# Kernel optimization log

Hardware: AMD Instinct MI355X
Metric: run time of the kernel (lower is better)

## Reference

```python
import jax, jax.numpy as jnp
import numpy as np
import math

PAD_IDX = 1
BOS_IDX = 2
B, S, T = 32, 128, 64
E, H, L, V = 256, 512, 2, 32000


def _lstm_cell(gates, c):
    # torch gate order: i, f, g, o
    i, f, g, o = jnp.split(gates, 4, axis=-1)
    c_new = jax.nn.sigmoid(f) * c + jax.nn.sigmoid(i) * jnp.tanh(g)
    h_new = jax.nn.sigmoid(o) * jnp.tanh(c_new)
    return h_new, c_new


def _run_lstm_layer(x_tbi, Wih, Whh, b, h0, c0):
    def step(carry, x_t):
        h, c = carry
        h2, c2 = _lstm_cell(x_t @ Wih + h @ Whh + b, c)
        return (h2, c2), h2
    (hT, cT), ys = jax.lax.scan(step, (h0, c0), x_tbi)
    return ys, hT, cT


def setup_inputs() -> dict:
    key = jax.random.key(0)
    ks = iter(jax.random.split(key, 40))
    def w(shape, s=0.05):
        return jax.random.normal(next(ks), shape, jnp.float32) * s
    inp = {
        'src_tokens': jax.random.randint(next(ks), (B, S), 0, V, dtype=jnp.int32),
        'tgt_tokens': jax.random.randint(next(ks), (B, T), 0, V, dtype=jnp.int32),
        'src_emb': w((V, E), 0.02),
        'tgt_emb': w((V, E), 0.02),
        'enc_Wih0': w((E, 4 * H)), 'enc_Whh0': w((H, 4 * H)), 'enc_b0': jnp.zeros((4 * H,), jnp.float32),
        'enc_Wih1': w((H, 4 * H)), 'enc_Whh1': w((H, 4 * H)), 'enc_b1': jnp.zeros((4 * H,), jnp.float32),
        'dec_Wih0': w((E + H, 4 * H)), 'dec_Whh0': w((H, 4 * H)), 'dec_b0': jnp.zeros((4 * H,), jnp.float32),
        'dec_Wih1': w((H, 4 * H)), 'dec_Whh1': w((H, 4 * H)), 'dec_b1': jnp.zeros((4 * H,), jnp.float32),
        'attn_W': w((2 * H, H)), 'attn_b': jnp.zeros((H,), jnp.float32),
        'v_w': w((H,)),
        'coal_w': w((L, 1), 0.5), 'coal_b': jnp.zeros((1,), jnp.float32),
        'out_W': w((2 * H + E, V)), 'out_b': jnp.zeros((V,), jnp.float32),
    }
    return inp


def reference(src_tokens, tgt_tokens, src_emb, tgt_emb,
              enc_Wih0, enc_Whh0, enc_b0, enc_Wih1, enc_Whh1, enc_b1,
              dec_Wih0, dec_Whh0, dec_b0, dec_Wih1, dec_Whh1, dec_b1,
              attn_W, attn_b, v_w, coal_w, coal_b, out_W, out_b):
    Bq = src_tokens.shape[0]
    sqrtE_src = np.float32(math.sqrt(src_emb.shape[1]))
    sqrtE_tgt = np.float32(math.sqrt(tgt_emb.shape[1]))

    # ---- Encoder (2-layer LSTM, batch_first; dropout=0 eval) ----
    x = (src_emb[src_tokens] * sqrtE_src).transpose(1, 0, 2)  # (S,B,E)
    z = jnp.zeros((Bq, H), jnp.float32)
    ys0, hA, cA = _run_lstm_layer(x, enc_Wih0, enc_Whh0, enc_b0, z, z)
    ys1, hB, cB = _run_lstm_layer(ys0, enc_Wih1, enc_Whh1, enc_b1, z, z)
    enc_out = ys1.transpose(1, 0, 2)          # (B,S,H)
    hidden = jnp.stack([hA, hB])              # (L,B,H)
    cell = jnp.stack([cA, cB])

    mask = src_tokens != PAD_IDX              # (B,S)
    Wq, We = attn_W[:H], attn_W[H:]
    enc_proj = enc_out @ We                   # (B,S,H) loop-invariant part of attn linear

    def dec_step(carry, tok):
        h, c = carry                          # (L,B,H) each
        emb = jax.nn.relu(tgt_emb[tok] * sqrtE_tgt)          # (B,E)
        # faithful raw reshape (L,B,H) -> (B,H,L), coalesce layers
        q = jax.nn.relu(h.reshape(Bq, H, L) @ coal_w + coal_b)[..., 0]  # (B,H)
        e = jnp.tanh(enc_proj + (q @ Wq + attn_b)[:, None, :])          # (B,S,H)
        score = e @ v_w                                                 # (B,S)
        score = jnp.where(mask, score, np.float32(-1e10))
        a = jax.nn.softmax(score, axis=1)
        wctx = jnp.einsum('bs,bsh->bh', a, enc_out)                     # (B,H)
        xin = jnp.concatenate([emb, wctx], axis=-1)                     # (B,E+H)
        h0n, c0n = _lstm_cell(xin @ dec_Wih0 + h[0] @ dec_Whh0 + dec_b0, c[0])
        h1n, c1n = _lstm_cell(h0n @ dec_Wih1 + h[1] @ dec_Whh1 + dec_b1, c[1])
        logits = jnp.concatenate([h1n, wctx, emb], axis=-1) @ out_W + out_b  # (B,V)
        return (jnp.stack([h0n, h1n]), jnp.stack([c0n, c1n])), logits

    (hF, cF), outs = jax.lax.scan(dec_step, (hidden, cell), tgt_tokens[:, :-1].T)
    first = jnp.full((Bq, 1, out_b.shape[0]), np.float32(BOS_IDX))  # decoder_outputs[:,0]=BOS_IDX
    dec_outputs = jnp.concatenate([first, outs.transpose(1, 0, 2)], axis=1)  # (B,T,V)
    return dec_outputs, hF, cF
```

## Files before the change

### kernel.cpp

```cpp
#include <hip/hip_runtime.h>
#include <hip/hip_bf16.h>

typedef __bf16 bf16x8 __attribute__((ext_vector_type(8)));
typedef float f32x4 __attribute__((ext_vector_type(4)));
typedef unsigned long long u64;

#define DEV static __device__ __forceinline__

constexpr int Bq = 32, Sq = 128, Tq = 64, Eq = 256, Hq = 512, Vq = 32000;
constexpr int G4 = 2048;
constexpr int TD = 63;
constexpr int KOUT = 1280;
constexpr float SQRTE = 16.0f;

DEV float sigf(float x) { return 1.0f / (1.0f + __expf(-x)); }
DEV float tanh_fast(float x) {
    float ax = fabsf(x);
    float t = __expf(-2.f * ax);
    float r = (1.f - t) / (1.f + t);
    return x < 0.f ? -r : r;
}
DEV float tanh_c(float x) {
    float xc = fminf(fmaxf(x, -15.f), 15.f);
    float t = __expf(2.f * xc);
    return (t - 1.f) / (t + 1.f);
}

DEV u64 ldc(const u64* p) {
    return __hip_atomic_load(p, __ATOMIC_RELAXED, __HIP_MEMORY_SCOPE_AGENT);
}
DEV unsigned ldc32(const unsigned* p) {
    return __hip_atomic_load(p, __ATOMIC_RELAXED, __HIP_MEMORY_SCOPE_AGENT);
}
DEV void stc(u64* p, u64 v) {
    __hip_atomic_store(p, v, __ATOMIC_RELAXED, __HIP_MEMORY_SCOPE_AGENT);
}
DEV void stc32(unsigned* p, unsigned v) {
    __hip_atomic_store(p, v, __ATOMIC_RELAXED, __HIP_MEMORY_SCOPE_AGENT);
}
DEV unsigned short bfbits(float f) {
    __bf16 h = (__bf16)f;
    return __builtin_bit_cast(unsigned short, h);
}
DEV float bf2f(unsigned short u) {
    __bf16 h = __builtin_bit_cast(__bf16, u);
    return (float)h;
}
DEV u64 pack4bf(float a, float b, float c, float d) {
    return (u64)bfbits(a) | ((u64)bfbits(b) << 16) |
           ((u64)bfbits(c) << 32) | ((u64)bfbits(d) << 48);
}
DEV u64 pack2f(float a, float b) {
    return (u64)__float_as_uint(a) | ((u64)__float_as_uint(b) << 32);
}

DEV void gbar(unsigned* flags, int nblk, unsigned epoch) {
    __syncthreads();
    if (threadIdx.x < 64) {
        if (threadIdx.x == 0) {
            asm volatile("s_waitcnt vmcnt(0)" ::: "memory");
            stc32(flags + blockIdx.x * 32, epoch);
        }
        int lane = threadIdx.x;
        for (;;) {
            unsigned v = (lane < nblk) ? ldc32(flags + lane * 32) : 0xffffffffu;
            if (__all((int)(v >= epoch))) break;
            __builtin_amdgcn_s_sleep(1);
        }
    }
    __syncthreads();
}

__global__ __launch_bounds__(256) void k_embed_src(const int* __restrict__ tok,
                                                   const float* __restrict__ emb,
                                                   __hip_bfloat16* __restrict__ x)
{
    int idx = blockIdx.x * 256 + threadIdx.x;
    int e = idx & (Eq - 1);
    int r = idx >> 8;
    int b = r & 31, t = r >> 5;
    x[idx] = __float2bfloat16(emb[(size_t)tok[b * Sq + t] * Eq + e] * SQRTE);
}

__global__ __launch_bounds__(256) void k_embed_tgt(const int* __restrict__ tok,
                                                   const float* __restrict__ emb,
                                                   __hip_bfloat16* __restrict__ embt,
                                                   __hip_bfloat16* __restrict__ Xout)
{
    int idx = blockIdx.x * 256 + threadIdx.x;
    int e = idx & (Eq - 1);
    int r = idx >> 8;
    int b = r & 31, t = r >> 5;
    float v = fmaxf(0.f, emb[(size_t)tok[b * Tq + t] * Eq + e] * SQRTE);
    embt[idx] = __float2bfloat16(v);
    Xout[(size_t)r * KOUT + 1024 + e] = __float2bfloat16(v);
}

__global__ __launch_bounds__(256) void k_transpose_bf16(const float* __restrict__ W,
                                                        __hip_bfloat16* __restrict__ Wt,
                                                        int K, int N)
{
    __shared__ float tile[32][33];
    int nb = blockIdx.x * 32, kb = blockIdx.y * 32;
    int c = threadIdx.x & 31, r4 = threadIdx.x >> 5;
    for (int i = 0; i < 32; i += 8)
        tile[r4 + i][c] = W[(size_t)(kb + r4 + i) * N + nb + c];
    __syncthreads();
    for (int i = 0; i < 32; i += 8) {
        int rr = r4 + i;
        Wt[(size_t)(nb + rr) * K + kb + c] = __float2bfloat16(tile[c][rr]);
    }
}

DEV void stage_coh(const u64* src, __bf16* As) {
    int tx = threadIdx.x;
#pragma unroll
    for (int p = 0; p < 8; ++p) {
        int c = tx + p * 256;
        int row = c >> 6, kc = c & 63;
        u64 v0 = ldc(src + c * 2);
        u64 v1 = ldc(src + c * 2 + 1);
        int kd = kc ^ (row & 7);
        *(u64*)(As + row * 512 + kd * 8) = v0;
        *(u64*)(As + row * 512 + kd * 8 + 4) = v1;
    }
}

DEV void mfma_pass(const __bf16* As, const unsigned short* BT, int colB,
                   int kg, int fr, f32x4* acc) {
    const unsigned short* bp = BT + (size_t)colB * 512 + kg * 8;
    int f7 = fr & 7;
#pragma unroll
    for (int k0 = 0; k0 < 512; k0 += 32) {
        int cidx = ((k0 >> 3) | kg) ^ f7;
        bf16x8 bfv = *(const bf16x8*)(bp + k0);
        bf16x8 af0 = *(const bf16x8*)(As + fr * 512 + cidx * 8);
        bf16x8 af1 = *(const bf16x8*)(As + (16 + fr) * 512 + cidx * 8);
        acc[0] = __builtin_amdgcn_mfma_f32_16x16x32_bf16(af0, bfv, acc[0], 0, 0, 0);
        acc[1] = __builtin_amdgcn_mfma_f32_16x16x32_bf16(af1, bfv, acc[1], 0, 0, 0);
    }
}

DEV void mfma_gates(const __bf16* As0, const __bf16* As1,
                    const __hip_bfloat16* B0T, const __hip_bfloat16* B1T,
                    int j0, float* gbuf)
{
    int tx = threadIdx.x, w = tx >> 6, lane = tx & 63;
    int fr = lane & 15, kg = lane >> 4;
    int colB = w * 512 + j0 + fr;
    f32x4 acc[2];
    acc[0] = (f32x4){0.f, 0.f, 0.f, 0.f};
    acc[1] = (f32x4){0.f, 0.f, 0.f, 0.f};
    mfma_pass(As0, (const unsigned short*)B0T, colB, kg, fr, acc);
    if (B1T) mfma_pass(As1, (const unsigned short*)B1T, colB, kg, fr, acc);
    __syncthreads();
    float* gw = gbuf + w * 512;
#pragma unroll
    for (int m = 0; m < 2; ++m)
#pragma unroll
        for (int qd = 0; qd < 4; ++qd)
            gw[(m * 16 + kg * 4 + qd) * 16 + fr] = acc[m][qd];
    __syncthreads();
}

DEV void cell_epi(const float* gbuf, const __hip_bfloat16* xpart, const float* bias,
                  float* cbuf, u64* hb, u64* hf,
                  __hip_bfloat16* eb, int ebs, bool ebcoh,
                  int j0)
{
    int tx = threadIdx.x;
    if (tx >= 128) return;
    int b = tx >> 2, jg = tx & 3;
    int jj0 = jg * 4;
    int j = j0 + jj0;
    float g[4][4];
#pragma unroll
    for (int gi = 0; gi < 4; ++gi) {
        float4 gv = *(const float4*)(gbuf + gi * 512 + b * 16 + jj0);
        g[gi][0] = gv.x; g[gi][1] = gv.y; g[gi][2] = gv.z; g[gi][3] = gv.w;
        if (xpart) {
            u64 xv = *(const u64*)((const unsigned short*)xpart + b * 2048 + gi * 512 + j);
#pragma unroll
            for (int e = 0; e < 4; ++e)
                g[gi][e] += bf2f((unsigned short)(xv >> (16 * e)));
        }
        if (bias) {
            float4 bv = *(const float4*)(bias + gi * 512 + j);
            g[gi][0] += bv.x; g[gi][1] += bv.y; g[gi][2] += bv.z; g[gi][3] += bv.w;
        }
    }
    float4 cv = *(float4*)(cbuf + b * 512 + j);
    float cc[4] = {cv.x, cv.y, cv.z, cv.w};
    float hv[4];
#pragma unroll
    for (int e = 0; e < 4; ++e) {
        float cn = sigf(g[1][e]) * cc[e] + sigf(g[0][e]) * tanh_fast(g[2][e]);
        cc[e] = cn;
        hv[e] = sigf(g[3][e]) * tanh_fast(cn);
    }
    *(float4*)(cbuf + b * 512 + j) = make_float4(cc[0], cc[1], cc[2], cc[3]);
    u64 hpk = pack4bf(hv[0], hv[1], hv[2], hv[3]);
    stc(hb + ((b * 512 + j) >> 2), hpk);
    stc(hf + ((b * 512 + j) >> 1), pack2f(hv[0], hv[1]));
    stc(hf + ((b * 512 + j) >> 1) + 1, pack2f(hv[2], hv[3]));
    if (eb) {
        if (ebcoh) stc((u64*)(eb + (size_t)b * ebs + j), hpk);
        else       *(u64*)(eb + (size_t)b * ebs + j) = hpk;
    }
}

__global__ __launch_bounds__(256) void k_enc_persist(
    const __hip_bfloat16* __restrict__ X0b,
    const __hip_bfloat16* __restrict__ eWhh0T, const __hip_bfloat16* __restrict__ eWih1T,
    const __hip_bfloat16* __restrict__ eWhh1T, const float* __restrict__ eb1,
    __hip_bfloat16* __restrict__ h0b, __hip_bfloat16* __restrict__ h1b,
    float* __restrict__ h0f, float* __restrict__ h1f,
    float* __restrict__ c0, float* __restrict__ c1,
    __hip_bfloat16* __restrict__ ys0b,
    __hip_bfloat16* __restrict__ encb,
    unsigned* __restrict__ flags)
{
    __shared__ __align__(16) char shm[65536];
    __bf16* As0 = (__bf16*)shm;
    __bf16* As1 = (__bf16*)(shm + 32768);
    bool lay1 = blockIdx.x >= 32;
    int j0 = (blockIdx.x & 31) * 16;
    for (int t = 0; t <= 128; ++t) {
        if (!lay1) {
            if (t < 128) {
                stage_coh((const u64*)(h0b + (t & 1) * 16384), As0);
                __syncthreads();
                mfma_gates(As0, nullptr, eWhh0T, nullptr, j0, (float*)As0);
                cell_epi((float*)As0, X0b + (size_t)t * 32 * 2048, nullptr,
                         c0, (u64*)(h0b + ((t + 1) & 1) * 16384), (u64*)h0f,
                         ys0b + (size_t)t * 16384, 512, true, j0);
            }
        } else {
            if (t >= 1) {
                int s = t - 1;
                stage_coh((const u64*)(ys0b + (size_t)s * 16384), As0);
                stage_coh((const u64*)(h1b + (s & 1) * 16384), As1);
                __syncthreads();
                mfma_gates(As0, As1, eWih1T, eWhh1T, j0, (float*)As0);
                cell_epi((float*)As0, nullptr, eb1,
                         c1, (u64*)(h1b + ((s + 1) & 1) * 16384), (u64*)h1f,
                         encb + s * 512, 128 * 512, false, j0);
            }
        }
        gbar(flags, 64, (unsigned)(t + 1));
    }
}

__global__ __launch_bounds__(256) void k_dec_persist(
    const __hip_bfloat16* __restrict__ enc_projb, const __hip_bfloat16* __restrict__ enc_outb,
    const int* __restrict__ src_tok, const float* __restrict__ v_w,
    const __hip_bfloat16* __restrict__ WqT, const float* __restrict__ attn_b,
    const float* __restrict__ coal_w, const float* __restrict__ coal_b,
    const __hip_bfloat16* __restrict__ dWih0wT, const __hip_bfloat16* __restrict__ dWhh0T,
    const __hip_bfloat16* __restrict__ dWih1T, const __hip_bfloat16* __restrict__ dWhh1T,
    const float* __restrict__ db1, const __hip_bfloat16* __restrict__ Xembb,
    float* __restrict__ h0fd, float* __restrict__ h1fd,
    __hip_bfloat16* __restrict__ h0bd, __hip_bfloat16* __restrict__ h1bd,
    float* __restrict__ c0d, float* __restrict__ c1d,
    __hip_bfloat16* __restrict__ wctxb,
    __hip_bfloat16* __restrict__ Xout,
    unsigned* __restrict__ flags)
{
    __shared__ __align__(16) char shm[65536];
    __shared__ float rinvs;
    __bf16* As0 = (__bf16*)shm;
    __bf16* As1 = (__bf16*)(shm + 32768);
    int bid = blockIdx.x, tx = threadIdx.x;
    unsigned bep = 0;

    for (int t = 0; t < TD; ++t) {
        int cur = t & 1, nxt = cur ^ 1;
        __hip_bfloat16* XoutT = Xout + (size_t)t * 32 * KOUT;

        {
            int b = bid;
            float* q   = (float*)shm;
            float* aqs = q + 512;
            float* vws = aqs + 512;
            float* ws  = vws + 512;
            const float* hrow = (b < 16) ? (h0fd + cur * 16384 + b * 1024)
                                         : (h1fd + cur * 16384 + (b - 16) * 1024);
            float cw0 = coal_w[0], cw1 = coal_w[1], cb = coal_b[0];
            for (int j = tx; j < 512; j += 256) {
                u64 pv = ldc((const u64*)hrow + j);
                float v0 = __uint_as_float((unsigned)(pv & 0xffffffffu));
                float v1 = __uint_as_float((unsigned)(pv >> 32));
                q[j] = fmaxf(0.f, v0 * cw0 + v1 * cw1 + cb);
            }
            for (int i = tx; i < 512; i += 256) vws[i] = v_w[i];
            __syncthreads();
            float a0 = attn_b[tx], a1 = attn_b[tx + 256];
            const unsigned short* w0 = (const unsigned short*)WqT + (size_t)tx * 512;
            const unsigned short* w1 = w0 + 256 * 512;
#pragma unroll 4
            for (int j8 = 0; j8 < 512; j8 += 8) {
                bf16x8 wa = *(const bf16x8*)(w0 + j8);
                bf16x8 wb = *(const bf16x8*)(w1 + j8);
#pragma unroll
                for (int e = 0; e < 8; ++e) {
                    float qe = q[j8 + e];
                    a0 += qe * (float)wa[e];
                    a1 += qe * (float)wb[e];
                }
            }
            aqs[tx] = a0; aqs[tx + 256] = a1;
            __syncthreads();
            int s = tx >> 1, half = tx & 1;
            const unsigned short* epr = (const unsigned short*)enc_projb
                                        + ((size_t)(b * 128 + s)) * 512 + half * 256;
            float s0 = 0.f, s1 = 0.f, s2 = 0.f, s3 = 0.f;
#pragma unroll 4
            for (int ii = 0; ii < 256; ii += 8) {
                bf16x8 f8 = *(const bf16x8*)(epr + ii);
                int ib = half * 256 + ii;
                s0 += tanh_c((float)f8[0] + aqs[ib])     * vws[ib];
                s1 += tanh_c((float)f8[1] + aqs[ib + 1]) * vws[ib + 1];
                s2 += tanh_c((float)f8[2] + aqs[ib + 2]) * vws[ib + 2];
                s3 += tanh_c((float)f8[3] + aqs[ib + 3]) * vws[ib + 3];
                s0 += tanh_c((float)f8[4] + aqs[ib + 4]) * vws[ib + 4];
                s1 += tanh_c((float)f8[5] + aqs[ib + 5]) * vws[ib + 5];
                s2 += tanh_c((float)f8[6] + aqs[ib + 6]) * vws[ib + 6];
                s3 += tanh_c((float)f8[7] + aqs[ib + 7]) * vws[ib + 7];
            }
            float p = (s0 + s1) + (s2 + s3);
            p += __shfl_xor(p, 1, 64);
            if (half == 0)
                ws[s] = (src_tok[b * 128 + s] != 1) ? __expf(p) : 0.f;
            __syncthreads();
            if (tx < 64) {
                float ss = ws[tx] + ws[tx + 64];
#pragma unroll
                for (int o = 32; o > 0; o >>= 1) ss += __shfl_down(ss, o, 64);
                if (tx == 0) rinvs = 1.0f / ss;
            }
            __syncthreads();
            float rinv = rinvs;
            const unsigned short* eo = (const unsigned short*)enc_outb + (size_t)b * 65536;
            int i0 = tx * 2;
            float c0a = 0.f, c1a = 0.f;
#pragma unroll 4
            for (int s2i = 0; s2i < 128; ++s2i) {
                unsigned pk2 = *(const unsigned*)(eo + (size_t)s2i * 512 + i0);
                float wv = ws[s2i];
                c0a += wv * bf2f((unsigned short)(pk2 & 0xffffu));
                c1a += wv * bf2f((unsigned short)(pk2 >> 16));
            }
            c0a *= rinv; c1a *= rinv;
            unsigned pk = (unsigned)bfbits(c0a) | ((unsigned)bfbits(c1a) << 16);
            stc32((unsigned*)wctxb + ((b * 512 + i0) >> 1), pk);
            *((unsigned*)XoutT + (((size_t)b * KOUT + 512 + i0) >> 1)) = pk;
        }
        gbar(flags, 32, ++bep);

        {
            int j0 = bid * 16;
            stage_coh((const u64*)wctxb, As0);
            stage_coh((const u64*)(h0bd + cur * 16384), As1);
            __syncthreads();
            mfma_gates(As0, As1, dWih0wT, dWhh0T, j0, (float*)As0);
            cell_epi((float*)As0, Xembb + (size_t)t * 32 * 2048, nullptr,
                     c0d, (u64*)(h0bd + nxt * 16384), (u64*)(h0fd + nxt * 16384),
                     nullptr, 0, false, j0);
        }
        gbar(flags, 32, ++bep);

        {
            int j0 = bid * 16;
            stage_coh((const u64*)(h0bd + nxt * 16384), As0);
            stage_coh((const u64*)(h1bd + cur * 16384), As1);
            __syncthreads();
            mfma_gates(As0, As1, dWih1T, dWhh1T, j0, (float*)As0);
            cell_epi((float*)As0, nullptr, db1,
                     c1d, (u64*)(h1bd + nxt * 16384), (u64*)(h1fd + nxt * 16384),
                     XoutT, KOUT, false, j0);
        }
        gbar(flags, 32, ++bep);
    }
}

__global__ __launch_bounds__(256) void k_mfma(
    const __hip_bfloat16* __restrict__ A, const __hip_bfloat16* __restrict__ BT,
    const float* __restrict__ bias, float* __restrict__ Cf,
    __hip_bfloat16* __restrict__ Cb, int M, int N, int K)
{
    __shared__ __bf16 As[128][72];
    __shared__ __bf16 Bs[128][72];
    const unsigned short* Aw = (const unsigned short*)A;
    const unsigned short* Bw = (const unsigned short*)BT;
    int n0 = blockIdx.x * 128, m0 = blockIdx.y * 128;
    int tx = threadIdx.x;
    int w = tx >> 6, lane = tx & 63;
    int wm = (w >> 1) * 64, wn = (w & 1) * 64;
    int fr = lane & 15, kg = lane >> 4;
    f32x4 acc[4][4];
#pragma unroll
    for (int mi = 0; mi < 4; mi++)
#pragma unroll
        for (int ni = 0; ni < 4; ni++) acc[mi][ni] = (f32x4){0.f, 0.f, 0.f, 0.f};

    for (int k0 = 0; k0 < K; k0 += 64) {
        __syncthreads();
#pragma unroll
        for (int p = 0; p < 4; p++) {
            int ch = tx + p * 256;
            int r = ch >> 3, cc = (ch & 7) * 8;
            uint4 va = {0u, 0u, 0u, 0u};
            int m = m0 + r;
            if (m < M) va = *(const uint4*)(Aw + (size_t)m * K + k0 + cc);
            *(uint4*)(&As[r][cc]) = va;
            uint4 vb = *(const uint4*)(Bw + (size_t)(n0 + r) * K + k0 + cc);
            *(uint4*)(&Bs[r][cc]) = vb;
        }
        __syncthreads();
#pragma unroll
        for (int kk = 0; kk < 64; kk += 32) {
            bf16x8 af[4], bfv[4];
#pragma unroll
            for (int i = 0; i < 4; i++) {
                af[i]  = *(const bf16x8*)(&As[wm + i * 16 + fr][kk + kg * 8]);
                bfv[i] = *(const bf16x8*)(&Bs[wn + i * 16 + fr][kk + kg * 8]);
            }
#pragma unroll
            for (int mi = 0; mi < 4; mi++)
#pragma unroll
                for (int ni = 0; ni < 4; ni++)
                    acc[mi][ni] = __builtin_amdgcn_mfma_f32_16x16x32_bf16(
                        af[mi], bfv[ni], acc[mi][ni], 0, 0, 0);
        }
    }
#pragma unroll
    for (int ni = 0; ni < 4; ni++) {
        int n = n0 + wn + ni * 16 + fr;
        float bv = bias ? bias[n] : 0.f;
#pragma unroll
        for (int mi = 0; mi < 4; mi++) {
#pragma unroll
            for (int qd = 0; qd < 4; qd++) {
                int R = m0 + wm + mi * 16 + kg * 4 + qd;
                if (R < M) {
                    float v = acc[mi][ni][qd] + bv;
                    if (Cf) Cf[(size_t)R * N + n] = v;
                    else    Cb[(size_t)R * N + n] = __float2bfloat16(v);
                }
            }
        }
    }
}

__global__ __launch_bounds__(256) void k_init_dec(
    const float* __restrict__ h0e, const float* __restrict__ h1e,
    const float* __restrict__ c0e, const float* __restrict__ c1e,
    float* __restrict__ h0fd, float* __restrict__ h1fd,
    __hip_bfloat16* __restrict__ h0bd, __hip_bfloat16* __restrict__ h1bd,
    float* __restrict__ c0d, float* __restrict__ c1d)
{
    int idx = blockIdx.x * 256 + threadIdx.x;
    float a = h0e[idx], b = h1e[idx];
    h0fd[idx] = a; h1fd[idx] = b;
    h0bd[idx] = __float2bfloat16(a);
    h1bd[idx] = __float2bfloat16(b);
    c0d[idx] = c0e[idx];
    c1d[idx] = c1e[idx];
}

__global__ __launch_bounds__(256) void k_bos(float* __restrict__ out)
{
    int b = blockIdx.y;
    int i = blockIdx.x * 256 + threadIdx.x;
    out[(size_t)b * (Tq * Vq) + i] = 2.0f;
}

__global__ __launch_bounds__(256) void k_finalize(
    const float* __restrict__ h0f, const float* __restrict__ h1f,
    const float* __restrict__ c0f, const float* __restrict__ c1f,
    float* __restrict__ out)
{
    int idx = blockIdx.x * 256 + threadIdx.x;
    size_t base = (size_t)Bq * Tq * Vq;
    out[base + idx] = h0f[idx];
    out[base + 16384 + idx] = h1f[idx];
    out[base + 32768 + idx] = c0f[idx];
    out[base + 49152 + idx] = c1f[idx];
}

__global__ __launch_bounds__(256) void k_logits(
    const __hip_bfloat16* __restrict__ A, const __hip_bfloat16* __restrict__ Bt,
    const float* __restrict__ bias, float* __restrict__ out)
{
    __shared__ __bf16 As[128][72];
    __shared__ __bf16 Bs[128][72];
    const unsigned short* Aw = (const unsigned short*)A;
    const unsigned short* Bw = (const unsigned short*)Bt;
    int n0 = blockIdx.x * 128, m0 = blockIdx.y * 128;
    int tx = threadIdx.x;
    int w = tx >> 6, lane = tx & 63;
    int wm = (w >> 1) * 64, wn = (w & 1) * 64;
    int fr = lane & 15, kg = lane >> 4;
    f32x4 acc[4][4];
#pragma unroll
    for (int mi = 0; mi < 4; mi++)
#pragma unroll
        for (int ni = 0; ni < 4; ni++) acc[mi][ni] = (f32x4){0.f, 0.f, 0.f, 0.f};

    for (int k0 = 0; k0 < 1280; k0 += 64) {
        __syncthreads();
#pragma unroll
        for (int p = 0; p < 4; p++) {
            int ch = tx + p * 256;
            int r = ch >> 3, cc = (ch & 7) * 8;
            uint4 va = {0u, 0u, 0u, 0u};
            int m = m0 + r;
            if (m < 2016) va = *(const uint4*)(Aw + (size_t)m * 1280 + k0 + cc);
            *(uint4*)(&As[r][cc]) = va;
            uint4 vb = *(const uint4*)(Bw + (size_t)(n0 + r) * 1280 + k0 + cc);
            *(uint4*)(&Bs[r][cc]) = vb;
        }
        __syncthreads();
#pragma unroll
        for (int kk = 0; kk < 64; kk += 32) {
            bf16x8 af[4], bfv[4];
#pragma unroll
            for (int i = 0; i < 4; i++) {
                af[i]  = *(const bf16x8*)(&As[wm + i * 16 + fr][kk + kg * 8]);
                bfv[i] = *(const bf16x8*)(&Bs[wn + i * 16 + fr][kk + kg * 8]);
            }
#pragma unroll
            for (int mi = 0; mi < 4; mi++)
#pragma unroll
                for (int ni = 0; ni < 4; ni++)
                    acc[mi][ni] = __builtin_amdgcn_mfma_f32_16x16x32_bf16(
                        af[mi], bfv[ni], acc[mi][ni], 0, 0, 0);
        }
    }
#pragma unroll
    for (int ni = 0; ni < 4; ni++) {
        int n = n0 + wn + ni * 16 + fr;
        float bv = bias[n];
#pragma unroll
        for (int mi = 0; mi < 4; mi++) {
#pragma unroll
            for (int qd = 0; qd < 4; qd++) {
                int R = m0 + wm + mi * 16 + kg * 4 + qd;
                if (R < 2016) {
                    int bb = R & 31, ts = R >> 5;
                    out[(size_t)bb * (Tq * Vq) + (size_t)(ts + 1) * Vq + n] =
                        acc[mi][ni][qd] + bv;
                }
            }
        }
    }
}

extern "C" void kernel_launch(void* const* d_in, const int* in_sizes, int n_in,
                              void* d_out, int out_size, void* d_ws, size_t ws_size,
                              hipStream_t stream)
{
    (void)in_sizes; (void)n_in; (void)out_size; (void)ws_size;
    const int*   src_tok = (const int*)  d_in[0];
    const int*   tgt_tok = (const int*)  d_in[1];
    const float* src_emb = (const float*)d_in[2];
    const float* tgt_emb = (const float*)d_in[3];
    const float* eWih0   = (const float*)d_in[4];
    const float* eWhh0   = (const float*)d_in[5];
    const float* eb0     = (const float*)d_in[6];
    const float* eWih1   = (const float*)d_in[7];
    const float* eWhh1   = (const float*)d_in[8];
    const float* eb1     = (const float*)d_in[9];
    const float* dWih0   = (const float*)d_in[10];
    const float* dWhh0   = (const float*)d_in[11];
    const float* db0     = (const float*)d_in[12];
    const float* dWih1   = (const float*)d_in[13];
    const float* dWhh1   = (const float*)d_in[14];
    const float* db1     = (const float*)d_in[15];
    const float* attn_W  = (const float*)d_in[16];
    const float* attn_b  = (const float*)d_in[17];
    const float* v_w     = (const float*)d_in[18];
    const float* coal_w  = (const float*)d_in[19];
    const float* coal_b  = (const float*)d_in[20];
    const float* out_W   = (const float*)d_in[21];
    const float* out_b   = (const float*)d_in[22];
    float* out = (float*)d_out;

    char* ws = (char*)d_ws;
    size_t off = 0;
    auto alloc = [&](size_t bytes) -> char* {
        char* p = ws + off;
        off += (bytes + 255) & ~(size_t)255;
        return p;
    };
    typedef __hip_bfloat16 BF;
    BF* X0b     = (BF*)alloc(4096ull * 2048 * 2);
    BF* Xembb   = (BF*)alloc(2016ull * 2048 * 2);
    BF* x_srcb  = (BF*)alloc(4096ull * 256 * 2);
    BF* embtb   = (BF*)alloc(2016ull * 256 * 2);
    BF* ys0b    = (BF*)alloc(128ull * 16384 * 2);
    BF* enc_outb  = (BF*)alloc(4096ull * 512 * 2);
    BF* enc_projb = (BF*)alloc(4096ull * 512 * 2);
    BF* wctxb     = (BF*)alloc(16384ull * 2);
    BF* Xout      = (BF*)alloc(2016ull * 1280 * 2);
    BF* Wt        = (BF*)alloc(32000ull * 1280 * 2);
    BF* eWhh0T  = (BF*)alloc(2048ull * 512 * 2);
    BF* eWih1T  = (BF*)alloc(2048ull * 512 * 2);
    BF* eWhh1T  = (BF*)alloc(2048ull * 512 * 2);
    BF* dWih0wT = (BF*)alloc(2048ull * 512 * 2);
    BF* dWhh0T  = (BF*)alloc(2048ull * 512 * 2);
    BF* dWih1T  = (BF*)alloc(2048ull * 512 * 2);
    BF* dWhh1T  = (BF*)alloc(2048ull * 512 * 2);
    BF* eWih0T  = (BF*)alloc(2048ull * 256 * 2);
    BF* dWih0eT = (BF*)alloc(2048ull * 256 * 2);
    BF* WqT     = (BF*)alloc(512ull * 512 * 2);
    BF* WeT     = (BF*)alloc(512ull * 512 * 2);
    BF* h0b_e   = (BF*)alloc(2ull * 16384 * 2);
    BF* h1b_e   = (BF*)alloc(2ull * 16384 * 2);
    float* h0f_e = (float*)alloc(16384ull * 4);
    float* h1f_e = (float*)alloc(16384ull * 4);
    float* c0e   = (float*)alloc(16384ull * 4);
    float* c1e   = (float*)alloc(16384ull * 4);
    float* h0fd  = (float*)alloc(2ull * 16384 * 4);
    float* h1fd  = (float*)alloc(2ull * 16384 * 4);
    BF* h0bd     = (BF*)alloc(2ull * 16384 * 2);
    BF* h1bd     = (BF*)alloc(2ull * 16384 * 2);
    float* c0d   = (float*)alloc(16384ull * 4);
    float* c1d   = (float*)alloc(16384ull * 4);
    unsigned* encFlags = (unsigned*)alloc(64 * 32 * 4);
    unsigned* decFlags = (unsigned*)alloc(32 * 32 * 4);

    hipMemsetAsync(encFlags, 0, 64 * 32 * 4, stream);
    hipMemsetAsync(decFlags, 0, 32 * 32 * 4, stream);
    hipMemsetAsync(h0b_e, 0, 2 * 16384 * 2, stream);
    hipMemsetAsync(h1b_e, 0, 2 * 16384 * 2, stream);
    hipMemsetAsync(c0e, 0, 16384 * 4, stream);
    hipMemsetAsync(c1e, 0, 16384 * 4, stream);

    k_embed_src<<<4096, 256, 0, stream>>>(src_tok, src_emb, x_srcb);
    k_embed_tgt<<<2016, 256, 0, stream>>>(tgt_tok, tgt_emb, embtb, Xout);

    k_transpose_bf16<<<dim3(64, 16), 256, 0, stream>>>(eWhh0, eWhh0T, 512, 2048);
    k_transpose_bf16<<<dim3(64, 16), 256, 0, stream>>>(eWih1, eWih1T, 512, 2048);
    k_transpose_bf16<<<dim3(64, 16), 256, 0, stream>>>(eWhh1, eWhh1T, 512, 2048);
    k_transpose_bf16<<<dim3(64, 16), 256, 0, stream>>>(dWih0 + 256 * 2048, dWih0wT, 512, 2048);
    k_transpose_bf16<<<dim3(64, 16), 256, 0, stream>>>(dWhh0, dWhh0T, 512, 2048);
    k_transpose_bf16<<<dim3(64, 16), 256, 0, stream>>>(dWih1, dWih1T, 512, 2048);
    k_transpose_bf16<<<dim3(64, 16), 256, 0, stream>>>(dWhh1, dWhh1T, 512, 2048);
    k_transpose_bf16<<<dim3(64, 8), 256, 0, stream>>>(eWih0, eWih0T, 256, 2048);
    k_transpose_bf16<<<dim3(64, 8), 256, 0, stream>>>(dWih0, dWih0eT, 256, 2048);
    k_transpose_bf16<<<dim3(16, 16), 256, 0, stream>>>(attn_W, WqT, 512, 512);
    k_transpose_bf16<<<dim3(16, 16), 256, 0, stream>>>(attn_W + 512 * 512, WeT, 512, 512);
    k_transpose_bf16<<<dim3(1000, 40), 256, 0, stream>>>(out_W, Wt, 1280, 32000);

    k_mfma<<<dim3(16, 32), 256, 0, stream>>>(x_srcb, eWih0T, eb0, nullptr, X0b, 4096, 2048, 256);
    k_mfma<<<dim3(16, 16), 256, 0, stream>>>(embtb, dWih0eT, db0, nullptr, Xembb, 2016, 2048, 256);
    k_bos<<<dim3(125, 32), 256, 0, stream>>>(out);

    k_enc_persist<<<64, 256, 0, stream>>>(X0b, eWhh0T, eWih1T, eWhh1T, eb1,
                                          h0b_e, h1b_e, h0f_e, h1f_e, c0e, c1e,
                                          ys0b, enc_outb, encFlags);

    k_mfma<<<dim3(4, 32), 256, 0, stream>>>(enc_outb, WeT, nullptr, nullptr, enc_projb, 4096, 512, 512);

    k_init_dec<<<64, 256, 0, stream>>>(h0f_e, h1f_e, c0e, c1e,
                                       h0fd, h1fd, h0bd, h1bd, c0d, c1d);

    k_dec_persist<<<32, 256, 0, stream>>>(enc_projb, enc_outb, src_tok, v_w,
                                          WqT, attn_b, coal_w, coal_b,
                                          dWih0wT, dWhh0T, dWih1T, dWhh1T,
                                          db1, Xembb,
                                          h0fd, h1fd, h0bd, h1bd, c0d, c1d,
                                          wctxb, Xout, decFlags);

    k_finalize<<<64, 256, 0, stream>>>(h0fd + (TD & 1) * 16384, h1fd + (TD & 1) * 16384,
                                       c0d, c1d, out);
    k_logits<<<dim3(250, 16), 256, 0, stream>>>(Xout, Wt, out_b, out);
}
```

Baseline: 5.560 ms.

## Split decoder recurrent Whh matmuls onto extra persistent blocks overlapping attention

The decoder persistent kernel grows from 32 to 96 blocks. The new blocks compute h@Whh for both layers into global slabs while the first 32 blocks run attention, and the cell epilogues then add the slab values. The attention query projection now reads fp32 attn_W directly with coalesced column access instead of a pre-transposed bf16 copy, which drops one transpose. The grid barrier now polls up to 128 flags per wave. This takes recurrent matmul work off the critical path, at the cost of a wider barrier and extra global round-trips for the gate partials.

Result: slower. 5.788 ms (+4.1%).

```diff
diff --git a/kernel.cpp b/kernel.cpp
--- a/kernel.cpp
+++ b/kernel.cpp
@@ -63,8 +63,9 @@
         }
         int lane = threadIdx.x;
         for (;;) {
-            unsigned v = (lane < nblk) ? ldc32(flags + lane * 32) : 0xffffffffu;
-            if (__all((int)(v >= epoch))) break;
+            unsigned v0 = (lane < nblk) ? ldc32(flags + lane * 32) : epoch;
+            unsigned v1 = (lane + 64 < nblk) ? ldc32(flags + (lane + 64) * 32) : epoch;
+            if (__all((int)((v0 >= epoch) && (v1 >= epoch)))) break;
             __builtin_amdgcn_s_sleep(1);
         }
     }
@@ -163,10 +164,31 @@
     __syncthreads();
 }
 
-DEV void cell_epi(const float* gbuf, const __hip_bfloat16* xpart, const float* bias,
+DEV void gh_pass(const u64* hsrc, const __hip_bfloat16* WT,
+                 float* slab_tile, int j0, __bf16* As0)
+{
+    stage_coh(hsrc, As0);
+    __syncthreads();
+    int tx = threadIdx.x, w = tx >> 6, lane = tx & 63;
+    int fr = lane & 15, kg = lane >> 4;
+    int colB = w * 512 + j0 + fr;
+    f32x4 acc[2];
+    acc[0] = (f32x4){0.f, 0.f, 0.f, 0.f};
+    acc[1] = (f32x4){0.f, 0.f, 0.f, 0.f};
+    mfma_pass(As0, (const unsigned short*)WT, colB, kg, fr, acc);
+    float* outp = slab_tile + w * 512;
+#pragma unroll
+    for (int m = 0; m < 2; ++m)
+#pragma unroll
+        for (int qd = 0; qd < 4; ++qd)
+            stc32((unsigned*)(outp + (m * 16 + kg * 4 + qd) * 16 + fr),
+                  __float_as_uint(acc[m][qd]));
+}
+
+DEV void cell_epi(const float* gbuf, const float* gadd,
+                  const __hip_bfloat16* xpart, const float* bias,
                   float* cbuf, u64* hb, u64* hf,
-                  __hip_bfloat16* eb, int ebs, bool ebcoh,
-                  int j0)
+                  __hip_bfloat16* eb, int ebs, int j0)
 {
     int tx = threadIdx.x;
     if (tx >= 128) return;
@@ -176,8 +198,17 @@
     float g[4][4];
 #pragma unroll
     for (int gi = 0; gi < 4; ++gi) {
-        float4 gv = *(const float4*)(gbuf + gi * 512 + b * 16 + jj0);
+        int idx = gi * 512 + b * 16 + jj0;
+        float4 gv = *(const float4*)(gbuf + idx);
         g[gi][0] = gv.x; g[gi][1] = gv.y; g[gi][2] = gv.z; g[gi][3] = gv.w;
+        if (gadd) {
+            u64 p0 = ldc((const u64*)gadd + (idx >> 1));
+            u64 p1 = ldc((const u64*)gadd + (idx >> 1) + 1);
+            g[gi][0] += __uint_as_float((unsigned)(p0 & 0xffffffffu));
+            g[gi][1] += __uint_as_float((unsigned)(p0 >> 32));
+            g[gi][2] += __uint_as_float((unsigned)(p1 & 0xffffffffu));
+            g[gi][3] += __uint_as_float((unsigned)(p1 >> 32));
+        }
         if (xpart) {
             u64 xv = *(const u64*)((const unsigned short*)xpart + b * 2048 + gi * 512 + j);
 #pragma unroll
@@ -203,10 +234,7 @@
     stc(hb + ((b * 512 + j) >> 2), hpk);
     stc(hf + ((b * 512 + j) >> 1), pack2f(hv[0], hv[1]));
     stc(hf + ((b * 512 + j) >> 1) + 1, pack2f(hv[2], hv[3]));
-    if (eb) {
-        if (ebcoh) stc((u64*)(eb + (size_t)b * ebs + j), hpk);
-        else       *(u64*)(eb + (size_t)b * ebs + j) = hpk;
-    }
+    if (eb) *(u64*)(eb + (size_t)b * ebs + j) = hpk;
 }
 
 __global__ __launch_bounds__(256) void k_enc_persist(
@@ -231,9 +259,15 @@
                 stage_coh((const u64*)(h0b + (t & 1) * 16384), As0);
                 __syncthreads();
                 mfma_gates(As0, nullptr, eWhh0T, nullptr, j0, (float*)As0);
-                cell_epi((float*)As0, X0b + (size_t)t * 32 * 2048, nullptr,
+                cell_epi((float*)As0, nullptr, X0b + (size_t)t * 32 * 2048, nullptr,
                          c0, (u64*)(h0b + ((t + 1) & 1) * 16384), (u64*)h0f,
-                         ys0b + (size_t)t * 16384, 512, true, j0);
+                         nullptr, 0, j0);
+                if (threadIdx.x < 128) {
+                    int b = threadIdx.x >> 2, jg = threadIdx.x & 3;
+                    int j = j0 + jg * 4;
+                    u64 hpk = ldc((const u64*)(h0b + ((t + 1) & 1) * 16384) + ((b * 512 + j) >> 2));
+                    stc((u64*)(ys0b + (size_t)t * 16384 + b * 512 + j), hpk);
+                }
             }
         } else {
             if (t >= 1) {
@@ -242,9 +276,9 @@
                 stage_coh((const u64*)(h1b + (s & 1) * 16384), As1);
                 __syncthreads();
                 mfma_gates(As0, As1, eWih1T, eWhh1T, j0, (float*)As0);
-                cell_epi((float*)As0, nullptr, eb1,
+                cell_epi((float*)As0, nullptr, nullptr, eb1,
                          c1, (u64*)(h1b + ((s + 1) & 1) * 16384), (u64*)h1f,
-                         encb + s * 512, 128 * 512, false, j0);
+                         encb + s * 512, 128 * 512, j0);
             }
         }
         gbar(flags, 64, (unsigned)(t + 1));
@@ -254,7 +288,7 @@
 __global__ __launch_bounds__(256) void k_dec_persist(
     const __hip_bfloat16* __restrict__ enc_projb, const __hip_bfloat16* __restrict__ enc_outb,
     const int* __restrict__ src_tok, const float* __restrict__ v_w,
-    const __hip_bfloat16* __restrict__ WqT, const float* __restrict__ attn_b,
+    const float* __restrict__ attn_W, const float* __restrict__ attn_b,
     const float* __restrict__ coal_w, const float* __restrict__ coal_b,
     const __hip_bfloat16* __restrict__ dWih0wT, const __hip_bfloat16* __restrict__ dWhh0T,
     const __hip_bfloat16* __restrict__ dWih1T, const __hip_bfloat16* __restrict__ dWhh1T,
@@ -264,12 +298,12 @@
     float* __restrict__ c0d, float* __restrict__ c1d,
     __hip_bfloat16* __restrict__ wctxb,
     __hip_bfloat16* __restrict__ Xout,
+    float* __restrict__ g0slab, float* __restrict__ g1slab,
     unsigned* __restrict__ flags)
 {
-    __shared__ __align__(16) char shm[65536];
+    __shared__ __align__(16) char shm[32768];
     __shared__ float rinvs;
     __bf16* As0 = (__bf16*)shm;
-    __bf16* As1 = (__bf16*)(shm + 32768);
     int bid = blockIdx.x, tx = threadIdx.x;
     unsigned bep = 0;
 
@@ -277,7 +311,7 @@
         int cur = t & 1, nxt = cur ^ 1;
         __hip_bfloat16* XoutT = Xout + (size_t)t * 32 * KOUT;
 
-        {
+        if (bid < 32) {
             int b = bid;
             float* q   = (float*)shm;
             float* aqs = q + 512;
@@ -295,18 +329,11 @@
             for (int i = tx; i < 512; i += 256) vws[i] = v_w[i];
             __syncthreads();
             float a0 = attn_b[tx], a1 = attn_b[tx + 256];
-            const unsigned short* w0 = (const unsigned short*)WqT + (size_t)tx * 512;
-            const unsigned short* w1 = w0 + 256 * 512;
-#pragma unroll 4
-            for (int j8 = 0; j8 < 512; j8 += 8) {
-                bf16x8 wa = *(const bf16x8*)(w0 + j8);
-                bf16x8 wb = *(const bf16x8*)(w1 + j8);
-#pragma unroll
-                for (int e = 0; e < 8; ++e) {
-                    float qe = q[j8 + e];
-                    a0 += qe * (float)wa[e];
-                    a1 += qe * (float)wb[e];
-                }
+#pragma unroll 8
+            for (int j = 0; j < 512; ++j) {
+                float qj = q[j];
+                a0 += qj * attn_W[(size_t)j * 512 + tx];
+                a1 += qj * attn_W[(size_t)j * 512 + tx + 256];
             }
             aqs[tx] = a0; aqs[tx + 256] = a1;
             __syncthreads();
@@ -354,32 +381,40 @@
             unsigned pk = (unsigned)bfbits(c0a) | ((unsigned)bfbits(c1a) << 16);
             stc32((unsigned*)wctxb + ((b * 512 + i0) >> 1), pk);
             *((unsigned*)XoutT + (((size_t)b * KOUT + 512 + i0) >> 1)) = pk;
-        }
-        gbar(flags, 32, ++bep);
-
-        {
+        } else if (bid < 64) {
+            int tile = bid - 32;
+            gh_pass((const u64*)(h0bd + cur * 16384), dWhh0T,
+                    g0slab + tile * 2048, tile * 16, As0);
+        } else {
+            int tile = bid - 64;
+            gh_pass((const u64*)(h1bd + cur * 16384), dWhh1T,
+                    g1slab + tile * 2048, tile * 16, As0);
+        }
+        gbar(flags, 96, ++bep);
+
+        if (bid < 32) {
             int j0 = bid * 16;
             stage_coh((const u64*)wctxb, As0);
-            stage_coh((const u64*)(h0bd + cur * 16384), As1);
             __syncthreads();
-            mfma_gates(As0, As1, dWih0wT, dWhh0T, j0, (float*)As0);
-            cell_epi((float*)As0, Xembb + (size_t)t * 32 * 2048, nullptr,
+            mfma_gates(As0, nullptr, dWih0wT, nullptr, j0, (float*)As0);
+            cell_epi((float*)As0, g0slab + bid * 2048,
+                     Xembb + (size_t)t * 32 * 2048, nullptr,
                      c0d, (u64*)(h0bd + nxt * 16384), (u64*)(h0fd + nxt * 16384),
-                     nullptr, 0, false, j0);
-        }
-        gbar(flags, 32, ++bep);
-
-        {
+                     nullptr, 0, j0);
+        }
+        gbar(flags, 96, ++bep);
+
+        if (bid < 32) {
             int j0 = bid * 16;
             stage_coh((const u64*)(h0bd + nxt * 16384), As0);
-            stage_coh((const u64*)(h1bd + cur * 16384), As1);
             __syncthreads();
-            mfma_gates(As0, As1, dWih1T, dWhh1T, j0, (float*)As0);
-            cell_epi((float*)As0, nullptr, db1,
+            mfma_gates(As0, nullptr, dWih1T, nullptr, j0, (float*)As0);
+            cell_epi((float*)As0, g1slab + bid * 2048,
+                     nullptr, db1,
                      c1d, (u64*)(h1bd + nxt * 16384), (u64*)(h1fd + nxt * 16384),
-                     XoutT, KOUT, false, j0);
-        }
-        gbar(flags, 32, ++bep);
+                     XoutT, KOUT, j0);
+        }
+        gbar(flags, 96, ++bep);
     }
 }
 
@@ -613,7 +648,6 @@
     BF* dWhh1T  = (BF*)alloc(2048ull * 512 * 2);
     BF* eWih0T  = (BF*)alloc(2048ull * 256 * 2);
     BF* dWih0eT = (BF*)alloc(2048ull * 256 * 2);
-    BF* WqT     = (BF*)alloc(512ull * 512 * 2);
     BF* WeT     = (BF*)alloc(512ull * 512 * 2);
     BF* h0b_e   = (BF*)alloc(2ull * 16384 * 2);
     BF* h1b_e   = (BF*)alloc(2ull * 16384 * 2);
@@ -627,11 +661,13 @@
     BF* h1bd     = (BF*)alloc(2ull * 16384 * 2);
     float* c0d   = (float*)alloc(16384ull * 4);
     float* c1d   = (float*)alloc(16384ull * 4);
+    float* g0slab = (float*)alloc(32ull * 2048 * 4);
+    float* g1slab = (float*)alloc(32ull * 2048 * 4);
     unsigned* encFlags = (unsigned*)alloc(64 * 32 * 4);
-    unsigned* decFlags = (unsigned*)alloc(32 * 32 * 4);
+    unsigned* decFlags = (unsigned*)alloc(96 * 32 * 4);
 
     hipMemsetAsync(encFlags, 0, 64 * 32 * 4, stream);
-    hipMemsetAsync(decFlags, 0, 32 * 32 * 4, stream);
+    hipMemsetAsync(decFlags, 0, 96 * 32 * 4, stream);
     hipMemsetAsync(h0b_e, 0, 2 * 16384 * 2, stream);
     hipMemsetAsync(h1b_e, 0, 2 * 16384 * 2, stream);
     hipMemsetAsync(c0e, 0, 16384 * 4, stream);
@@ -649,7 +685,6 @@
     k_transpose_bf16<<<dim3(64, 16), 256, 0, stream>>>(dWhh1, dWhh1T, 512, 2048);
     k_transpose_bf16<<<dim3(64, 8), 256, 0, stream>>>(eWih0, eWih0T, 256, 2048);
     k_transpose_bf16<<<dim3(64, 8), 256, 0, stream>>>(dWih0, dWih0eT, 256, 2048);
-    k_transpose_bf16<<<dim3(16, 16), 256, 0, stream>>>(attn_W, WqT, 512, 512);
     k_transpose_bf16<<<dim3(16, 16), 256, 0, stream>>>(attn_W + 512 * 512, WeT, 512, 512);
     k_transpose_bf16<<<dim3(1000, 40), 256, 0, stream>>>(out_W, Wt, 1280, 32000);
 
@@ -666,12 +701,12 @@
     k_init_dec<<<64, 256, 0, stream>>>(h0f_e, h1f_e, c0e, c1e,
                                        h0fd, h1fd, h0bd, h1bd, c0d, c1d);
 
-    k_dec_persist<<<32, 256, 0, stream>>>(enc_projb, enc_outb, src_tok, v_w,
-                                          WqT, attn_b, coal_w, coal_b,
+    k_dec_persist<<<96, 256, 0, stream>>>(enc_projb, enc_outb, src_tok, v_w,
+                                          attn_W, attn_b, coal_w, coal_b,
                                           dWih0wT, dWhh0T, dWih1T, dWhh1T,
                                           db1, Xembb,
                                           h0fd, h1fd, h0bd, h1bd, c0d, c1d,
-                                          wctxb, Xout, decFlags);
+                                          wctxb, Xout, g0slab, g1slab, decFlags);
 
     k_finalize<<<64, 256, 0, stream>>>(h0fd + (TD & 1) * 16384, h1fd + (TD & 1) * 16384,
                                        c0d, c1d, out);
```
